# Kernel tuning notes

Hardware: AMD Instinct MI355X
Metric: run time of the kernel (lower is better)

The kernel has to match this reference:

```python
import jax, jax.numpy as jnp
import numpy as np


def setup_inputs() -> dict:
    key = jax.random.key(0)
    k1, k2, k3, k4, k5 = jax.random.split(key, 5)
    B, S, H = 64, 2048, 512
    enc = jax.random.normal(k1, (B, S, H), dtype=jnp.float32)
    fin = jax.random.normal(k2, (B, H), dtype=jnp.float32)
    # nn.Linear(2H, H): weight [H, 2H]; nn.Linear(H, 1, bias=False): weight [1, H]
    attn_w = jax.random.normal(k3, (H, 2 * H), dtype=jnp.float32) * (1.0 / np.sqrt(2 * H))
    attn_b = jax.random.normal(k4, (H,), dtype=jnp.float32) * 0.01
    v_w = jax.random.normal(k5, (1, H), dtype=jnp.float32) * (1.0 / np.sqrt(H))
    return {"encoder_outputs": enc, "final_hidden": fin,
            "attn_w": attn_w, "attn_b": attn_b, "v_w": v_w}


def reference(encoder_outputs, final_hidden, attn_w, attn_b, v_w):
    # Split attn_w into the encoder part and final-hidden part to avoid
    # materializing the [B, S, 2H] concat tensor (same math as concat+linear).
    H = final_hidden.shape[-1]
    w_enc = attn_w[:, :H]   # [H, H]
    w_fin = attn_w[:, H:]   # [H, H]
    # energy: [B, S, H]
    e_enc = jnp.einsum('bsh,kh->bsk', encoder_outputs, w_enc)
    e_fin = jnp.einsum('bh,kh->bk', final_hidden, w_fin)
    energy = jnp.tanh(e_enc + e_fin[:, None, :] + attn_b)
    scores = jnp.einsum('bsk,k->bs', energy, v_w[0])      # [B, S]
    weights = jax.nn.softmax(scores, axis=1)              # [B, S]
    context = jnp.einsum('bs,bsh->bh', weights, encoder_outputs)  # [B, H]
    return context
```

## Files before the change

### kernel.cpp

```cpp
#include <hip/hip_runtime.h>
#include <hip/hip_bf16.h>

#define BATCH 64
#define SEQ   2048
#define HID   512
#define ROWS  (BATCH * SEQ)

typedef __attribute__((ext_vector_type(8))) short short8;
typedef __attribute__((ext_vector_type(4))) float f32x4;

#define GLOBAL_AS __attribute__((address_space(1)))
#define LDS_AS    __attribute__((address_space(3)))

__device__ __forceinline__ void g2l16(const void* g, void* l) {
    __builtin_amdgcn_global_load_lds((const GLOBAL_AS unsigned int*)g,
                                     (LDS_AS unsigned int*)l, 16, 0, 0);
}

__device__ inline unsigned int cvt2_bf16(float x, float y) {
    __hip_bfloat162 h = __float22bfloat162_rn(make_float2(x, y));
    union { __hip_bfloat162 h2; unsigned int u; } u;
    u.h2 = h;
    return u.u;
}

__device__ inline float fast_tanh(float x) {
    float e = __expf(2.0f * x);
    return 1.0f - 2.0f / (e + 1.0f);
}

__device__ inline float bf16lo(unsigned int u) { return __uint_as_float(u << 16); }
__device__ inline float bf16hi(unsigned int u) { return __uint_as_float(u & 0xffff0000u); }

#define PREP_GRID 33920
__global__ void k_prep(const float* __restrict__ enc, const float* __restrict__ attw,
                       const float* __restrict__ attb, const float* __restrict__ fin,
                       unsigned short* __restrict__ encb, unsigned short* __restrict__ wb,
                       float* __restrict__ cbuf) {
    int bid = blockIdx.x;
    int t   = threadIdx.x;
    if (bid < 32768) {
        size_t i = ((size_t)bid * 256 + t) * 8;
        float4 a0 = *(const float4*)(enc + i);
        float4 a1 = *(const float4*)(enc + i + 4);
        uint4 p = {cvt2_bf16(a0.x, a0.y), cvt2_bf16(a0.z, a0.w),
                   cvt2_bf16(a1.x, a1.y), cvt2_bf16(a1.z, a1.w)};
        *(uint4*)(encb + i) = p;
    } else if (bid < 32896) {
        size_t e = ((size_t)(bid - 32768) * 256 + t) * 8;
        int k = (int)(e >> 9);
        int h = (int)(e & 511);
        const float* g = attw + (size_t)k * (2 * HID) + h;
        float4 a0 = *(const float4*)g;
        float4 a1 = *(const float4*)(g + 4);
        uint4 p = {cvt2_bf16(a0.x, a0.y), cvt2_bf16(a0.z, a0.w),
                   cvt2_bf16(a1.x, a1.y), cvt2_bf16(a1.z, a1.w)};
        *(uint4*)(wb + (size_t)k * HID + h) = p;
    } else {
        int fb = bid - 32896;
        int b  = fb >> 4;
        int k  = (fb & 15) * 32 + (t >> 3);
        int l8 = t & 7;
        const float* f = fin + b * HID;
        const float* w = attw + (size_t)k * (2 * HID) + HID;
        float s = 0.0f;
        for (int h = l8 * 4; h < HID; h += 32) {
            float4 a  = *(const float4*)(f + h);
            float4 ww = *(const float4*)(w + h);
            s += a.x * ww.x + a.y * ww.y + a.z * ww.z + a.w * ww.w;
        }
        s += __shfl_xor(s, 1);
        s += __shfl_xor(s, 2);
        s += __shfl_xor(s, 4);
        if (l8 == 0) cbuf[b * HID + k] = s + attb[k];
    }
}

__global__ __launch_bounds__(256, 2) void k_energy4(
        const unsigned short* __restrict__ encb, const unsigned short* __restrict__ wb,
        const float* __restrict__ cbuf, const float* __restrict__ vw,
        float* __restrict__ sp) {
    __shared__ __align__(16) unsigned short As[128 * 64];
    __shared__ __align__(16) unsigned short Bs[2 * 128 * 64];
    __shared__ float ssc[128];

    const int nBase = blockIdx.x * 256;
    const int sRow  = blockIdx.y * 128;
    const int bIdx  = sRow >> 11;

    const int t    = threadIdx.x;
    const int lane = t & 63;
    const int wave = t >> 6;
    const int wm   = wave >> 1;
    const int wn   = wave & 1;
    const int l16  = lane & 15;
    const int q    = lane >> 4;

    const int lr = lane >> 3;
    const int lc = lane & 7;
    const int sw = lc ^ lr;

    const unsigned short* gA  = encb + (size_t)(sRow + wave * 32 + lr) * HID + sw * 8;
    const unsigned short* gB0 = wb   + (size_t)(nBase + wave * 32 + lr) * HID + sw * 8;
    const unsigned short* gB1 = wb   + (size_t)(nBase + 128 + wave * 32 + lr) * HID + sw * 8;

    f32x4 acc0[4][4], acc1[4][4];
    #pragma unroll
    for (int i = 0; i < 4; ++i)
        #pragma unroll
        for (int j = 0; j < 4; ++j) {
            acc0[i][j] = (f32x4){0.f, 0.f, 0.f, 0.f};
            acc1[i][j] = (f32x4){0.f, 0.f, 0.f, 0.f};
        }

    for (int h0 = 0; h0 < HID; h0 += 64) {
        #pragma unroll
        for (int j = 0; j < 4; ++j) {
            g2l16(gA  + (size_t)(j * 8) * HID + h0, As + (wave * 32 + j * 8) * 64);
            g2l16(gB0 + (size_t)(j * 8) * HID + h0, Bs + (wave * 32 + j * 8) * 64);
            g2l16(gB1 + (size_t)(j * 8) * HID + h0, Bs + (128 + wave * 32 + j * 8) * 64);
        }
        __syncthreads();

        #pragma unroll
        for (int kk = 0; kk < 64; kk += 32) {
            short8 af[4], bf0[4], bf1[4];
            #pragma unroll
            for (int i = 0; i < 4; ++i) {
                int row = wm * 64 + i * 16 + l16;
                int c   = (kk >> 3) + q;
                af[i] = *(const short8*)(&As[row * 64 + (c ^ (row & 7)) * 8]);
            }
            #pragma unroll
            for (int j = 0; j < 4; ++j) {
                int row = wn * 64 + j * 16 + l16;
                int c   = (kk >> 3) + q;
                bf0[j] = *(const short8*)(&Bs[row * 64 + (c ^ (row & 7)) * 8]);
                bf1[j] = *(const short8*)(&Bs[(128 + row) * 64 + (c ^ (row & 7)) * 8]);
            }
            #pragma unroll
            for (int i = 0; i < 4; ++i)
                #pragma unroll
                for (int j = 0; j < 4; ++j) {
                    acc0[i][j] = __builtin_amdgcn_mfma_f32_16x16x32_bf16(
                        af[i], bf0[j], acc0[i][j], 0, 0, 0);
                    acc1[i][j] = __builtin_amdgcn_mfma_f32_16x16x32_bf16(
                        af[i], bf1[j], acc1[i][j], 0, 0, 0);
                }
        }
        __syncthreads();
    }

    if (t < 128) ssc[t] = 0.0f;
    __syncthreads();

    float cv0[4], vv0[4], cv1[4], vv1[4];
    #pragma unroll
    for (int j = 0; j < 4; ++j) {
        int c0 = nBase + wn * 64 + j * 16 + l16;
        int c1 = c0 + 128;
        cv0[j] = cbuf[bIdx * HID + c0];
        vv0[j] = vw[c0];
        cv1[j] = cbuf[bIdx * HID + c1];
        vv1[j] = vw[c1];
    }

    #pragma unroll
    for (int i = 0; i < 4; ++i) {
        #pragma unroll
        for (int r = 0; r < 4; ++r) {
            float sum = 0.0f;
            #pragma unroll
            for (int j = 0; j < 4; ++j) {
                sum += fast_tanh(acc0[i][j][r] + cv0[j]) * vv0[j];
                sum += fast_tanh(acc1[i][j][r] + cv1[j]) * vv1[j];
            }
            sum += __shfl_xor(sum, 1);
            sum += __shfl_xor(sum, 2);
            sum += __shfl_xor(sum, 4);
            sum += __shfl_xor(sum, 8);
            if (l16 == 0)
                atomicAdd(&ssc[wm * 64 + i * 16 + q * 4 + r], sum);
        }
    }
    __syncthreads();
    if (t < 128) sp[(size_t)blockIdx.x * ROWS + sRow + t] = ssc[t];
}

__global__ void k_context4(const unsigned short* __restrict__ encb,
                           const float* __restrict__ sp, float* __restrict__ out) {
    int b  = blockIdx.y;
    int sc = blockIdx.x;
    int t  = threadIdx.x;
    __shared__ float red[4];
    __shared__ float w[256];

    const float* p = sp + (size_t)b * SEQ;

    float lmax = -1e30f;
    float loc[8];
    #pragma unroll
    for (int k = 0; k < 8; ++k) {
        int i = k * 256 + t;
        float v = p[i] + p[i + ROWS];
        loc[k] = v;
        lmax = fmaxf(lmax, v);
    }
    for (int m = 1; m < 64; m <<= 1) lmax = fmaxf(lmax, __shfl_xor(lmax, m));
    if ((t & 63) == 0) red[t >> 6] = lmax;
    __syncthreads();
    float gmax = fmaxf(fmaxf(red[0], red[1]), fmaxf(red[2], red[3]));
    __syncthreads();

    float lsum = 0.0f;
    #pragma unroll
    for (int k = 0; k < 8; ++k) lsum += __expf(loc[k] - gmax);
    for (int m = 1; m < 64; m <<= 1) lsum += __shfl_xor(lsum, m);
    if ((t & 63) == 0) red[t >> 6] = lsum;
    __syncthreads();
    float inv = 1.0f / (red[0] + red[1] + red[2] + red[3]);

    {
        int i = sc * 256 + t;
        float v = p[i] + p[i + ROWS];
        w[t] = __expf(v - gmax) * inv;
    }
    __syncthreads();

    const unsigned short* e = encb + ((size_t)b * SEQ + sc * 256) * HID + t * 2;
    float ax = 0.0f, ay = 0.0f;
    #pragma unroll 8
    for (int s = 0; s < 256; ++s) {
        float ws = w[s];
        unsigned int v = *(const unsigned int*)(e + (size_t)s * HID);
        ax += ws * bf16lo(v);
        ay += ws * bf16hi(v);
    }
    atomicAdd(&out[b * HID + t * 2], ax);
    atomicAdd(&out[b * HID + t * 2 + 1], ay);
}

#define BK  64
#define LDA 72

__global__ __launch_bounds__(256) void k_energy_fb(
        const float* __restrict__ enc, const float* __restrict__ attw,
        const float* __restrict__ cbuf, const float* __restrict__ vw,
        float* __restrict__ scores) {
    __shared__ __align__(16) unsigned short As[128 * LDA];
    __shared__ __align__(16) unsigned short Bs[128 * LDA];
    const int nTile = blockIdx.x * 128;
    const int sRow  = blockIdx.y * 128;
    const int bIdx  = sRow >> 11;
    const int t = threadIdx.x, lane = t & 63, wave = t >> 6;
    const int wm = wave >> 1, wn = wave & 1, l16 = lane & 15, q = lane >> 4;
    const int tr = t >> 3, tc = (t & 7) * 8;

    f32x4 acc[4][4];
    #pragma unroll
    for (int i = 0; i < 4; ++i)
        #pragma unroll
        for (int j = 0; j < 4; ++j) acc[i][j] = (f32x4){0.f, 0.f, 0.f, 0.f};

    for (int h0 = 0; h0 < HID; h0 += BK) {
        #pragma unroll
        for (int i = 0; i < 4; ++i) {
            int row = tr + i * 32;
            const float* gA = enc + (size_t)(sRow + row) * HID + h0 + tc;
            float4 a0 = *(const float4*)gA;
            float4 a1 = *(const float4*)(gA + 4);
            uint4 pa = {cvt2_bf16(a0.x, a0.y), cvt2_bf16(a0.z, a0.w),
                        cvt2_bf16(a1.x, a1.y), cvt2_bf16(a1.z, a1.w)};
            *(uint4*)(&As[row * LDA + tc]) = pa;
            const float* gB = attw + (size_t)(nTile + row) * (2 * HID) + h0 + tc;
            float4 b0 = *(const float4*)gB;
            float4 b1 = *(const float4*)(gB + 4);
            uint4 pb = {cvt2_bf16(b0.x, b0.y), cvt2_bf16(b0.z, b0.w),
                        cvt2_bf16(b1.x, b1.y), cvt2_bf16(b1.z, b1.w)};
            *(uint4*)(&Bs[row * LDA + tc]) = pb;
        }
        __syncthreads();
        #pragma unroll
        for (int kk = 0; kk < BK; kk += 32) {
            short8 af[4], bf[4];
            #pragma unroll
            for (int i = 0; i < 4; ++i)
                af[i] = *(const short8*)(&As[(wm * 64 + i * 16 + l16) * LDA + kk + q * 8]);
            #pragma unroll
            for (int j = 0; j < 4; ++j)
                bf[j] = *(const short8*)(&Bs[(wn * 64 + j * 16 + l16) * LDA + kk + q * 8]);
            #pragma unroll
            for (int i = 0; i < 4; ++i)
                #pragma unroll
                for (int j = 0; j < 4; ++j)
                    acc[i][j] = __builtin_amdgcn_mfma_f32_16x16x32_bf16(
                        af[i], bf[j], acc[i][j], 0, 0, 0);
        }
        __syncthreads();
    }
    #pragma unroll
    for (int i = 0; i < 4; ++i) {
        #pragma unroll
        for (int r = 0; r < 4; ++r) {
            float sum = 0.0f;
            #pragma unroll
            for (int j = 0; j < 4; ++j) {
                int colg = nTile + wn * 64 + j * 16 + l16;
                sum += fast_tanh(acc[i][j][r] + cbuf[bIdx * HID + colg]) * vw[colg];
            }
            sum += __shfl_xor(sum, 1);
            sum += __shfl_xor(sum, 2);
            sum += __shfl_xor(sum, 4);
            sum += __shfl_xor(sum, 8);
            if (l16 == 0) atomicAdd(&scores[sRow + wm * 64 + i * 16 + q * 4 + r], sum);
        }
    }
}

__global__ void k_softmax(float* __restrict__ sw) {
    int b = blockIdx.x;
    float* s = sw + (size_t)b * SEQ;
    int t = threadIdx.x;
    __shared__ float red[4];
    float lmax = -1e30f;
    for (int i = t; i < SEQ; i += 256) lmax = fmaxf(lmax, s[i]);
    for (int m = 1; m < 64; m <<= 1) lmax = fmaxf(lmax, __shfl_xor(lmax, m));
    if ((t & 63) == 0) red[t >> 6] = lmax;
    __syncthreads();
    float gmax = fmaxf(fmaxf(red[0], red[1]), fmaxf(red[2], red[3]));
    __syncthreads();
    float lsum = 0.0f;
    for (int i = t; i < SEQ; i += 256) lsum += __expf(s[i] - gmax);
    for (int m = 1; m < 64; m <<= 1) lsum += __shfl_xor(lsum, m);
    if ((t & 63) == 0) red[t >> 6] = lsum;
    __syncthreads();
    float inv = 1.0f / (red[0] + red[1] + red[2] + red[3]);
    for (int i = t; i < SEQ; i += 256) s[i] = __expf(s[i] - gmax) * inv;
}

__global__ void k_fin_fb(const float* __restrict__ fin, const float* __restrict__ attw,
                         const float* __restrict__ attb, float* __restrict__ cbuf) {
    int b  = blockIdx.y;
    int k  = blockIdx.x * 32 + (threadIdx.x >> 3);
    int l8 = threadIdx.x & 7;
    const float* f = fin + b * HID;
    const float* w = attw + (size_t)k * (2 * HID) + HID;
    float s = 0.0f;
    for (int h = l8 * 4; h < HID; h += 32) {
        float4 a  = *(const float4*)(f + h);
        float4 ww = *(const float4*)(w + h);
        s += a.x * ww.x + a.y * ww.y + a.z * ww.z + a.w * ww.w;
    }
    s += __shfl_xor(s, 1);
    s += __shfl_xor(s, 2);
    s += __shfl_xor(s, 4);
    if (l8 == 0) cbuf[b * HID + k] = s + attb[k];
}

__global__ void k_context_fb(const float* __restrict__ enc, const float* __restrict__ wts,
                             float* __restrict__ out) {
    int b = blockIdx.y, sc = blockIdx.x, t = threadIdx.x;
    const float* e = enc + ((size_t)b * SEQ + sc * 128) * HID + t * 2;
    const float* w = wts + (size_t)b * SEQ + sc * 128;
    float ax = 0.f, ay = 0.f;
    #pragma unroll 4
    for (int s = 0; s < 128; ++s) {
        float ws = w[s];
        float2 v = *(const float2*)(e + (size_t)s * HID);
        ax += ws * v.x;
        ay += ws * v.y;
    }
    atomicAdd(&out[b * HID + t * 2], ax);
    atomicAdd(&out[b * HID + t * 2 + 1], ay);
}

extern "C" void kernel_launch(void* const* d_in, const int* in_sizes, int n_in,
                              void* d_out, int out_size, void* d_ws, size_t ws_size,
                              hipStream_t stream) {
    const float* enc  = (const float*)d_in[0];
    const float* fin  = (const float*)d_in[1];
    const float* attw = (const float*)d_in[2];
    const float* attb = (const float*)d_in[3];
    const float* vw   = (const float*)d_in[4];
    float* out = (float*)d_out;

    char* ws = (char*)d_ws;
    float* cbuf = (float*)ws;
    float* sp   = (float*)(ws + 131072);
    unsigned short* wb   = (unsigned short*)(ws + 131072 + 2 * 524288);
    unsigned short* encb = (unsigned short*)(ws + 131072 + 3 * 524288);
    const size_t need = 131072ull + 3 * 524288 + 134217728;

    hipMemsetAsync(out, 0, (size_t)BATCH * HID * sizeof(float), stream);

    if (ws_size >= need) {
        k_prep<<<PREP_GRID, 256, 0, stream>>>(enc, attw, attb, fin, encb, wb, cbuf);
        k_energy4<<<dim3(2, ROWS / 128), 256, 0, stream>>>(encb, wb, cbuf, vw, sp);
        k_context4<<<dim3(8, 64), 256, 0, stream>>>(encb, sp, out);
    } else {
        hipMemsetAsync(sp, 0, (size_t)ROWS * sizeof(float), stream);
        k_fin_fb<<<dim3(16, 64), 256, 0, stream>>>(fin, attw, attb, cbuf);
        k_energy_fb<<<dim3(4, ROWS / 128), 256, 0, stream>>>(enc, attw, cbuf, vw, sp);
        k_softmax<<<BATCH, 256, 0, stream>>>(sp);
        k_context_fb<<<dim3(16, 64), 256, 0, stream>>>(enc, sp, out);
    }
}
```

Baseline: 502.0 us.

## Fuse bf16 conversion, energy GEMM, local softmax and context into one pass

Removes the separate pass that converts the whole encoder tensor to bf16. The energy kernel now loads fp32 encoder rows, converts them in registers into LDS, and computes all 512 output columns per 64-row tile, so each row's score finishes inside one block. That block then computes a local softmax (max and sum) and a partial weighted context from the fp32 rows, which are still cache-hot. A small combine kernel merges the 32 partials per batch flash-style, replacing the atomics and the memset. The cost is that the full 512x64 weight tile is reloaded into LDS for every 64-row block, and the context pass rereads the fp32 rows.

```diff
diff --git a/kernel.cpp b/kernel.cpp
--- a/kernel.cpp
+++ b/kernel.cpp
@@ -29,25 +29,13 @@
     return 1.0f - 2.0f / (e + 1.0f);
 }
 
-__device__ inline float bf16lo(unsigned int u) { return __uint_as_float(u << 16); }
-__device__ inline float bf16hi(unsigned int u) { return __uint_as_float(u & 0xffff0000u); }
-
-#define PREP_GRID 33920
-__global__ void k_prep(const float* __restrict__ enc, const float* __restrict__ attw,
-                       const float* __restrict__ attb, const float* __restrict__ fin,
-                       unsigned short* __restrict__ encb, unsigned short* __restrict__ wb,
-                       float* __restrict__ cbuf) {
+__global__ void k_prep2(const float* __restrict__ attw, const float* __restrict__ attb,
+                        const float* __restrict__ fin, unsigned short* __restrict__ wb,
+                        float* __restrict__ cbuf) {
     int bid = blockIdx.x;
     int t   = threadIdx.x;
-    if (bid < 32768) {
-        size_t i = ((size_t)bid * 256 + t) * 8;
-        float4 a0 = *(const float4*)(enc + i);
-        float4 a1 = *(const float4*)(enc + i + 4);
-        uint4 p = {cvt2_bf16(a0.x, a0.y), cvt2_bf16(a0.z, a0.w),
-                   cvt2_bf16(a1.x, a1.y), cvt2_bf16(a1.z, a1.w)};
-        *(uint4*)(encb + i) = p;
-    } else if (bid < 32896) {
-        size_t e = ((size_t)(bid - 32768) * 256 + t) * 8;
+    if (bid < 128) {
+        size_t e = ((size_t)bid * 256 + t) * 8;
         int k = (int)(e >> 9);
         int h = (int)(e & 511);
         const float* g = attw + (size_t)k * (2 * HID) + h;
@@ -57,7 +45,7 @@
                    cvt2_bf16(a1.x, a1.y), cvt2_bf16(a1.z, a1.w)};
         *(uint4*)(wb + (size_t)k * HID + h) = p;
     } else {
-        int fb = bid - 32896;
+        int fb = bid - 128;
         int b  = fb >> 4;
         int k  = (fb & 15) * 32 + (t >> 3);
         int l8 = t & 7;
@@ -76,93 +64,90 @@
     }
 }
 
-__global__ __launch_bounds__(256, 2) void k_energy4(
-        const unsigned short* __restrict__ encb, const unsigned short* __restrict__ wb,
+__global__ __launch_bounds__(256, 2) void k_energy_f(
+        const float* __restrict__ enc, const unsigned short* __restrict__ wb,
         const float* __restrict__ cbuf, const float* __restrict__ vw,
-        float* __restrict__ sp) {
-    __shared__ __align__(16) unsigned short As[128 * 64];
-    __shared__ __align__(16) unsigned short Bs[2 * 128 * 64];
-    __shared__ float ssc[128];
-
-    const int nBase = blockIdx.x * 256;
-    const int sRow  = blockIdx.y * 128;
-    const int bIdx  = sRow >> 11;
-
+        float* __restrict__ num, float* __restrict__ ml) {
+    __shared__ __align__(16) unsigned short As[64 * 64];
+    __shared__ __align__(16) unsigned short Bs[512 * 64];
+
+    const int sRow = blockIdx.x * 64;
+    const int bIdx = sRow >> 11;
     const int t    = threadIdx.x;
     const int lane = t & 63;
     const int wave = t >> 6;
-    const int wm   = wave >> 1;
-    const int wn   = wave & 1;
     const int l16  = lane & 15;
     const int q    = lane >> 4;
 
-    const int lr = lane >> 3;
-    const int lc = lane & 7;
-    const int sw = lc ^ lr;
-
-    const unsigned short* gA  = encb + (size_t)(sRow + wave * 32 + lr) * HID + sw * 8;
-    const unsigned short* gB0 = wb   + (size_t)(nBase + wave * 32 + lr) * HID + sw * 8;
-    const unsigned short* gB1 = wb   + (size_t)(nBase + 128 + wave * 32 + lr) * HID + sw * 8;
-
-    f32x4 acc0[4][4], acc1[4][4];
+    const int tr = t >> 2;
+    const int tc = (t & 3) * 16;
+    const int c0 = (t & 3) * 2;
+
+    const int lr  = lane >> 3;
+    const int lc  = lane & 7;
+    const int swz = lc ^ lr;
+
+    const float* gA = enc + (size_t)(sRow + tr) * HID + tc;
+    const unsigned short* gB = wb + (size_t)(wave * 128 + lr) * HID + swz * 8;
+
+    f32x4 acc[4][8];
     #pragma unroll
     for (int i = 0; i < 4; ++i)
         #pragma unroll
-        for (int j = 0; j < 4; ++j) {
-            acc0[i][j] = (f32x4){0.f, 0.f, 0.f, 0.f};
-            acc1[i][j] = (f32x4){0.f, 0.f, 0.f, 0.f};
-        }
+        for (int j = 0; j < 8; ++j) acc[i][j] = (f32x4){0.f, 0.f, 0.f, 0.f};
 
     for (int h0 = 0; h0 < HID; h0 += 64) {
-        #pragma unroll
-        for (int j = 0; j < 4; ++j) {
-            g2l16(gA  + (size_t)(j * 8) * HID + h0, As + (wave * 32 + j * 8) * 64);
-            g2l16(gB0 + (size_t)(j * 8) * HID + h0, Bs + (wave * 32 + j * 8) * 64);
-            g2l16(gB1 + (size_t)(j * 8) * HID + h0, Bs + (128 + wave * 32 + j * 8) * 64);
-        }
+        float4 a0 = *(const float4*)(gA + h0);
+        float4 a1 = *(const float4*)(gA + h0 + 4);
+        float4 a2 = *(const float4*)(gA + h0 + 8);
+        float4 a3 = *(const float4*)(gA + h0 + 12);
+        #pragma unroll
+        for (int j = 0; j < 16; ++j)
+            g2l16(gB + (size_t)(j * 8) * HID + h0, Bs + (wave * 128 + j * 8) * 64);
+        uint4 p0 = {cvt2_bf16(a0.x, a0.y), cvt2_bf16(a0.z, a0.w),
+                    cvt2_bf16(a1.x, a1.y), cvt2_bf16(a1.z, a1.w)};
+        uint4 p1 = {cvt2_bf16(a2.x, a2.y), cvt2_bf16(a2.z, a2.w),
+                    cvt2_bf16(a3.x, a3.y), cvt2_bf16(a3.z, a3.w)};
+        *(uint4*)(&As[tr * 64 + ((c0    ) ^ (tr & 7)) * 8]) = p0;
+        *(uint4*)(&As[tr * 64 + ((c0 + 1) ^ (tr & 7)) * 8]) = p1;
         __syncthreads();
 
         #pragma unroll
         for (int kk = 0; kk < 64; kk += 32) {
-            short8 af[4], bf0[4], bf1[4];
+            short8 af[4], bf[8];
+            const int cb = (kk >> 3) + q;
             #pragma unroll
             for (int i = 0; i < 4; ++i) {
-                int row = wm * 64 + i * 16 + l16;
-                int c   = (kk >> 3) + q;
-                af[i] = *(const short8*)(&As[row * 64 + (c ^ (row & 7)) * 8]);
+                int row = i * 16 + l16;
+                af[i] = *(const short8*)(&As[row * 64 + (cb ^ (row & 7)) * 8]);
             }
             #pragma unroll
-            for (int j = 0; j < 4; ++j) {
-                int row = wn * 64 + j * 16 + l16;
-                int c   = (kk >> 3) + q;
-                bf0[j] = *(const short8*)(&Bs[row * 64 + (c ^ (row & 7)) * 8]);
-                bf1[j] = *(const short8*)(&Bs[(128 + row) * 64 + (c ^ (row & 7)) * 8]);
+            for (int j = 0; j < 8; ++j) {
+                int row = wave * 128 + j * 16 + l16;
+                bf[j] = *(const short8*)(&Bs[row * 64 + (cb ^ (row & 7)) * 8]);
             }
             #pragma unroll
             for (int i = 0; i < 4; ++i)
                 #pragma unroll
-                for (int j = 0; j < 4; ++j) {
-                    acc0[i][j] = __builtin_amdgcn_mfma_f32_16x16x32_bf16(
-                        af[i], bf0[j], acc0[i][j], 0, 0, 0);
-                    acc1[i][j] = __builtin_amdgcn_mfma_f32_16x16x32_bf16(
-                        af[i], bf1[j], acc1[i][j], 0, 0, 0);
-                }
+                for (int j = 0; j < 8; ++j)
+                    acc[i][j] = __builtin_amdgcn_mfma_f32_16x16x32_bf16(
+                        af[i], bf[j], acc[i][j], 0, 0, 0);
         }
         __syncthreads();
     }
 
-    if (t < 128) ssc[t] = 0.0f;
-    __syncthreads();
-
-    float cv0[4], vv0[4], cv1[4], vv1[4];
-    #pragma unroll
-    for (int j = 0; j < 4; ++j) {
-        int c0 = nBase + wn * 64 + j * 16 + l16;
-        int c1 = c0 + 128;
-        cv0[j] = cbuf[bIdx * HID + c0];
-        vv0[j] = vw[c0];
-        cv1[j] = cbuf[bIdx * HID + c1];
-        vv1[j] = vw[c1];
+    float* ssc = (float*)As;
+    float* wsm = (float*)As + 64;
+
+    if (t < 64) ssc[t] = 0.0f;
+    __syncthreads();
+
+    float cv[8], vv[8];
+    #pragma unroll
+    for (int j = 0; j < 8; ++j) {
+        int c = wave * 128 + j * 16 + l16;
+        cv[j] = cbuf[bIdx * HID + c];
+        vv[j] = vw[c];
     }
 
     #pragma unroll
@@ -171,73 +156,76 @@
         for (int r = 0; r < 4; ++r) {
             float sum = 0.0f;
             #pragma unroll
-            for (int j = 0; j < 4; ++j) {
-                sum += fast_tanh(acc0[i][j][r] + cv0[j]) * vv0[j];
-                sum += fast_tanh(acc1[i][j][r] + cv1[j]) * vv1[j];
-            }
+            for (int j = 0; j < 8; ++j)
+                sum += fast_tanh(acc[i][j][r] + cv[j]) * vv[j];
             sum += __shfl_xor(sum, 1);
             sum += __shfl_xor(sum, 2);
             sum += __shfl_xor(sum, 4);
             sum += __shfl_xor(sum, 8);
-            if (l16 == 0)
-                atomicAdd(&ssc[wm * 64 + i * 16 + q * 4 + r], sum);
-        }
-    }
-    __syncthreads();
-    if (t < 128) sp[(size_t)blockIdx.x * ROWS + sRow + t] = ssc[t];
-}
-
-__global__ void k_context4(const unsigned short* __restrict__ encb,
-                           const float* __restrict__ sp, float* __restrict__ out) {
-    int b  = blockIdx.y;
-    int sc = blockIdx.x;
-    int t  = threadIdx.x;
-    __shared__ float red[4];
-    __shared__ float w[256];
-
-    const float* p = sp + (size_t)b * SEQ;
-
-    float lmax = -1e30f;
-    float loc[8];
-    #pragma unroll
-    for (int k = 0; k < 8; ++k) {
-        int i = k * 256 + t;
-        float v = p[i] + p[i + ROWS];
-        loc[k] = v;
-        lmax = fmaxf(lmax, v);
-    }
-    for (int m = 1; m < 64; m <<= 1) lmax = fmaxf(lmax, __shfl_xor(lmax, m));
-    if ((t & 63) == 0) red[t >> 6] = lmax;
-    __syncthreads();
-    float gmax = fmaxf(fmaxf(red[0], red[1]), fmaxf(red[2], red[3]));
-    __syncthreads();
-
-    float lsum = 0.0f;
-    #pragma unroll
-    for (int k = 0; k < 8; ++k) lsum += __expf(loc[k] - gmax);
-    for (int m = 1; m < 64; m <<= 1) lsum += __shfl_xor(lsum, m);
-    if ((t & 63) == 0) red[t >> 6] = lsum;
-    __syncthreads();
-    float inv = 1.0f / (red[0] + red[1] + red[2] + red[3]);
-
-    {
-        int i = sc * 256 + t;
-        float v = p[i] + p[i + ROWS];
-        w[t] = __expf(v - gmax) * inv;
-    }
-    __syncthreads();
-
-    const unsigned short* e = encb + ((size_t)b * SEQ + sc * 256) * HID + t * 2;
+            if (l16 == 0) atomicAdd(&ssc[i * 16 + q * 4 + r], sum);
+        }
+    }
+    __syncthreads();
+
+    if (t < 64) {
+        float x  = ssc[t];
+        float mx = x;
+        #pragma unroll
+        for (int m = 1; m < 64; m <<= 1) mx = fmaxf(mx, __shfl_xor(mx, m));
+        float p = __expf(x - mx);
+        float l = p;
+        #pragma unroll
+        for (int m = 1; m < 64; m <<= 1) l += __shfl_xor(l, m);
+        wsm[t] = p;
+        if (t == 0) ((float2*)ml)[blockIdx.x] = make_float2(mx, l);
+    }
+    __syncthreads();
+
+    const float* e2 = enc + (size_t)sRow * HID + t * 2;
     float ax = 0.0f, ay = 0.0f;
     #pragma unroll 8
-    for (int s = 0; s < 256; ++s) {
-        float ws = w[s];
-        unsigned int v = *(const unsigned int*)(e + (size_t)s * HID);
-        ax += ws * bf16lo(v);
-        ay += ws * bf16hi(v);
-    }
-    atomicAdd(&out[b * HID + t * 2], ax);
-    atomicAdd(&out[b * HID + t * 2 + 1], ay);
+    for (int s = 0; s < 64; ++s) {
+        float p  = wsm[s];
+        float2 v = *(const float2*)(e2 + (size_t)s * HID);
+        ax += p * v.x;
+        ay += p * v.y;
+    }
+    *(float2*)(num + (size_t)blockIdx.x * HID + t * 2) = make_float2(ax, ay);
+}
+
+__global__ void k_combine(const float* __restrict__ num, const float* __restrict__ ml,
+                          float* __restrict__ out) {
+    int b = blockIdx.x;
+    int t = threadIdx.x;
+    __shared__ float sm[32], sl[32], sc[32];
+    __shared__ float sM;
+    if (t < 32) {
+        float2 v = ((const float2*)ml)[b * 32 + t];
+        sm[t] = v.x;
+        sl[t] = v.y;
+    }
+    __syncthreads();
+    if (t == 0) {
+        float M = -1e30f;
+        for (int i = 0; i < 32; ++i) M = fmaxf(M, sm[i]);
+        sM = M;
+    }
+    __syncthreads();
+    if (t < 32) sc[t] = __expf(sm[t] - sM);
+    __syncthreads();
+    float L = 0.0f;
+    #pragma unroll
+    for (int i = 0; i < 32; ++i) L += sc[i] * sl[i];
+    float inv = 1.0f / L;
+    const float* n = num + (size_t)b * 32 * HID + t;
+    float a0 = 0.0f, a1 = 0.0f;
+    #pragma unroll
+    for (int i = 0; i < 32; ++i) {
+        a0 += sc[i] * n[(size_t)i * HID];
+        a1 += sc[i] * n[(size_t)i * HID + 256];
+    }
+    out[b * HID + t]       = a0 * inv;
+    out[b * HID + t + 256] = a1 * inv;
 }
 
 #define BK  64
@@ -385,19 +373,19 @@
     float* out = (float*)d_out;
 
     char* ws = (char*)d_ws;
-    float* cbuf = (float*)ws;
-    float* sp   = (float*)(ws + 131072);
-    unsigned short* wb   = (unsigned short*)(ws + 131072 + 2 * 524288);
-    unsigned short* encb = (unsigned short*)(ws + 131072 + 3 * 524288);
-    const size_t need = 131072ull + 3 * 524288 + 134217728;
-
-    hipMemsetAsync(out, 0, (size_t)BATCH * HID * sizeof(float), stream);
+    float* cbuf        = (float*)ws;
+    unsigned short* wb = (unsigned short*)(ws + 131072);
+    float* num         = (float*)(ws + 131072 + 524288);
+    float* mlb         = (float*)(ws + 131072 + 524288 + 4194304);
+    const size_t need = 131072ull + 524288 + 4194304 + 16384;
 
     if (ws_size >= need) {
-        k_prep<<<PREP_GRID, 256, 0, stream>>>(enc, attw, attb, fin, encb, wb, cbuf);
-        k_energy4<<<dim3(2, ROWS / 128), 256, 0, stream>>>(encb, wb, cbuf, vw, sp);
-        k_context4<<<dim3(8, 64), 256, 0, stream>>>(encb, sp, out);
+        k_prep2<<<1152, 256, 0, stream>>>(attw, attb, fin, wb, cbuf);
+        k_energy_f<<<ROWS / 64, 256, 0, stream>>>(enc, wb, cbuf, vw, num, mlb);
+        k_combine<<<BATCH, 256, 0, stream>>>(num, mlb, out);
     } else {
+        float* sp = (float*)(ws + 131072);
+        hipMemsetAsync(out, 0, (size_t)BATCH * HID * sizeof(float), stream);
         hipMemsetAsync(sp, 0, (size_t)ROWS * sizeof(float), stream);
         k_fin_fb<<<dim3(16, 64), 256, 0, stream>>>(fin, attw, attb, cbuf);
         k_energy_fb<<<dim3(4, ROWS / 128), 256, 0, stream>>>(enc, attw, cbuf, vw, sp);
```

Measured after the change: 443.5 us. -11.6%, faster.
